# Optimization experiments

Measured on AMD Instinct MI355X. Metric: run time of the kernel, lower is better.

## Reference

```python
import jax, jax.numpy as jnp
import numpy as np

QUANT_DEPTH = 4
EMBED_DIM = 256
N_EMBED = 8192
B, H, W = 8, 32, 32


def setup_inputs() -> dict:
    key = jax.random.key(0)
    k1, k2 = jax.random.split(key)
    x = jax.random.normal(k1, (B, H, W, EMBED_DIM), dtype=jnp.float32)
    codebooks = jax.random.normal(k2, (QUANT_DEPTH, N_EMBED, EMBED_DIM), dtype=jnp.float32)
    return {"x": x, "codebooks": codebooks}


def _nearest_code(flat, cb):
    # flat: [N, D], cb: [K, D] -> idx: [N]
    # ||v - c||^2 = ||v||^2 + ||c||^2 - 2 v.c  (addmm in torch source)
    d = (jnp.sum(flat * flat, axis=1, keepdims=True)
         + jnp.sum(cb * cb, axis=1)[None, :]
         - 2.0 * (flat @ cb.T))  # [N, K]
    return jnp.argmin(d, axis=1)


def reference(x, codebooks):
    Bx, h, w, D = x.shape
    # quantization path is entirely non-differentiable (torch: detach + no_grad)
    resid = jax.lax.stop_gradient(x)
    agg = jnp.zeros_like(resid)
    quant_list = []
    code_list = []
    for i in range(codebooks.shape[0]):
        cb = codebooks[i]                      # [K, D]
        idx = _nearest_code(resid.reshape(-1, D), cb)  # [N]
        quant = cb[idx].reshape(Bx, h, w, D)
        resid = resid - quant
        agg = agg + quant
        quant_list.append(agg)
        code_list.append(idx.reshape(Bx, h, w, 1))
    codes = jnp.concatenate(code_list, axis=-1)  # [B, h, w, depth]
    # commitment loss: mean over depths of mean((x - agg_i.detach())^2)
    commitment_loss = jnp.mean(
        jnp.stack([jnp.mean((x - jax.lax.stop_gradient(q)) ** 2) for q in quant_list]))
    # straight-through estimator
    quants_trunc = x + jax.lax.stop_gradient(quant_list[-1] - x)
    return quants_trunc, commitment_loss, codes
```

## Files before the change

### kernel.cpp

```cpp
#include <hip/hip_runtime.h>

#define DIM   256
#define NVEC  8192
#define NCODE 8192
#define DEPTH 4

#define KBLK  8
#define KC    (NCODE / KBLK)
#define KT    (KC / 128)
#define FCAP  8192
#define FKS   32
#define FV    8
#define KAPPA 0.025f

typedef short  b8 __attribute__((ext_vector_type(8)));
typedef short  b4 __attribute__((ext_vector_type(4)));
typedef float  f4 __attribute__((ext_vector_type(4)));

static __device__ __forceinline__ unsigned short f2bf(float f) {
  unsigned u = __float_as_uint(f);
  return (unsigned short)((u + 0x7FFFu + ((u >> 16) & 1u)) >> 16);
}

static __device__ __forceinline__ void gll16(const void* g, void* l) {
  __builtin_amdgcn_global_load_lds(
      (const __attribute__((address_space(1))) void*)g,
      (__attribute__((address_space(3))) void*)l, 16, 0, 0);
}

__global__ __launch_bounds__(256) void prep_norms(const float* __restrict__ cb_all,
                                                  float* __restrict__ cc,
                                                  float* __restrict__ cchat) {
  int row  = blockIdx.x * 4 + (threadIdx.x >> 6);
  int lane = threadIdx.x & 63;
  float4 v = *(const float4*)&cb_all[(size_t)row * DIM + lane * 4];
  float st = 0.f, sh = 0.f;
  float vv[4] = {v.x, v.y, v.z, v.w};
  #pragma unroll
  for (int j = 0; j < 4; ++j) {
    float hf = __uint_as_float(((unsigned)f2bf(vv[j])) << 16);
    st += vv[j] * vv[j];
    sh += hf * hf;
  }
  #pragma unroll
  for (int off = 32; off > 0; off >>= 1) {
    st += __shfl_down(st, off, 64);
    sh += __shfl_down(sh, off, 64);
  }
  if (lane == 0) { cc[row] = st; cchat[row] = sh; }
}

__global__ __launch_bounds__(256) void prep_depth(const float* __restrict__ cbd,
                                                  unsigned short* __restrict__ cbh,
                                                  float* __restrict__ cbT) {
  __shared__ float ts[64][68];
  const int kb = blockIdx.x >> 2, db = blockIdx.x & 3;
  const int k0 = kb * 64, d0 = db * 64;
  const int t  = threadIdx.x;
  const int r  = t >> 2;
  const int c4 = (t & 3) * 16;

  const float* src = cbd + (size_t)(k0 + r) * DIM + d0 + c4;
  float4 q[4];
  #pragma unroll
  for (int i = 0; i < 4; ++i) q[i] = *(const float4*)(src + i * 4);

  b8 h0, h1;
  #pragma unroll
  for (int j = 0; j < 4; ++j) { h0[j] = (short)f2bf(q[0][j]); h0[4 + j] = (short)f2bf(q[1][j]); }
  #pragma unroll
  for (int j = 0; j < 4; ++j) { h1[j] = (short)f2bf(q[2][j]); h1[4 + j] = (short)f2bf(q[3][j]); }
  *(b8*)&cbh[(size_t)(k0 + r) * DIM + d0 + c4]     = h0;
  *(b8*)&cbh[(size_t)(k0 + r) * DIM + d0 + c4 + 8] = h1;

  #pragma unroll
  for (int i = 0; i < 4; ++i)
    #pragma unroll
    for (int j = 0; j < 4; ++j)
      ts[c4 + i * 4 + j][r] = q[i][j];
  __syncthreads();

  const int dd = t >> 2, kk4 = (t & 3) * 16;
  float* dst = cbT + (size_t)(d0 + dd) * NCODE + k0 + kk4;
  #pragma unroll
  for (int q4 = 0; q4 < 4; ++q4)
    *(float4*)(dst + q4 * 4) = *(const float4*)&ts[dd][kk4 + q4 * 4];
}

__global__ __launch_bounds__(256) void init_kernel(const float* __restrict__ x,
                                                   float* __restrict__ resid,
                                                   unsigned short* __restrict__ rb,
                                                   float* __restrict__ rsum0) {
  int n    = blockIdx.x * 4 + (threadIdx.x >> 6);
  int lane = threadIdx.x & 63;
  float4 v = *(const float4*)&x[(size_t)n * DIM + lane * 4];
  *(float4*)&resid[(size_t)n * DIM + lane * 4] = v;
  b4 hv; hv[0] = (short)f2bf(v.x); hv[1] = (short)f2bf(v.y);
  hv[2] = (short)f2bf(v.z); hv[3] = (short)f2bf(v.w);
  *(b4*)&rb[(size_t)n * DIM + lane * 4] = hv;
  float s = v.x * v.x + v.y * v.y + v.z * v.z + v.w * v.w;
  #pragma unroll
  for (int off = 32; off > 0; off >>= 1) s += __shfl_down(s, off, 64);
  if (lane == 0) rsum0[n] = s;
}

__global__ __launch_bounds__(512, 2) void coarse_kernel(
    const unsigned short* __restrict__ rb,
    const unsigned short* __restrict__ cbh,
    const float* __restrict__ cchat,
    float* __restrict__ pv1, int* __restrict__ pi1, float* __restrict__ pv2,
    int* __restrict__ fcount) {
  __shared__ __align__(16) char lds[53248];

  const int tid  = threadIdx.x;
  const int w    = tid >> 6;
  const int l    = tid & 63;
  const int mw   = w >> 1, kw = w & 1;
  const int mblk = blockIdx.x / KBLK;
  const int kblk = blockIdx.x % KBLK;
  const int m0   = mblk * 128;
  const int K0   = kblk * KC;

  if (blockIdx.x == 0 && tid == 0) *fcount = 0;

  int boff[2], ldst[2];
  #pragma unroll
  for (int it = 0; it < 2; ++it) {
    int o = it * 512 + tid;
    int row = o >> 3, ssl = (o & 7) ^ (row & 7);
    boff[it] = (K0 + row) * 512 + ssl * 16;
    ldst[it] = o * 16;
  }
  int offB[4][2];
  #pragma unroll
  for (int nf = 0; nf < 4; ++nf) {
    int row = kw * 64 + nf * 16 + (l & 15);
    int base = row * 128 + (((l >> 4) ^ (row & 7)) * 16);
    offB[nf][0] = base; offB[nf][1] = base ^ 64;
  }

  b8 ar[4][2][2];
  {
    const char* ab = (const char*)rb +
        (size_t)(m0 + mw * 32 + (l & 15)) * 512 + (l >> 4) * 16;
    #pragma unroll
    for (int dt = 0; dt < 4; ++dt)
      #pragma unroll
      for (int kk = 0; kk < 2; ++kk)
        #pragma unroll
        for (int mf = 0; mf < 2; ++mf)
          ar[dt][kk][mf] =
              *(const b8*)(ab + mf * (16 * 512) + dt * 128 + kk * 64);
  }
  if (tid < 256)
    gll16((const char*)cchat + (size_t)K0 * 4 + tid * 16,
          lds + 49152 + tid * 16);

  asm volatile("s_waitcnt vmcnt(0)");
  __builtin_amdgcn_sched_barrier(0);

  #pragma unroll
  for (int s = 0; s < 2; ++s)
    #pragma unroll
    for (int it = 0; it < 2; ++it)
      gll16((const char*)cbh + boff[it] + (s >> 2) * 65536 + (s & 3) * 128,
            lds + (s % 3) * 16384 + ldst[it]);

  const float* ccl = (const float*)(lds + 49152);
  const int kgb = K0 + kw * 64 + (l & 15);

  float tv1[8], tv2[8];
  int   ti1[8];
  #pragma unroll
  for (int s = 0; s < 8; ++s) { tv1[s] = 3.4e38f; tv2[s] = 3.4e38f; ti1[s] = 0; }

  f4 acc[2][4];

  #pragma unroll
  for (int p = 0; p < 32; ++p) {
    const int kt = p >> 2, dt = p & 3, cb_ = p % 3;
    if (p == 31) { asm volatile("s_waitcnt vmcnt(0)"); }
    else         { asm volatile("s_waitcnt vmcnt(2)"); }
    __builtin_amdgcn_s_barrier();
    __builtin_amdgcn_sched_barrier(0);
    if (p < 30) {
      const int s2 = p + 2, nb = s2 % 3, nkt = s2 >> 2, ndt = s2 & 3;
      #pragma unroll
      for (int it = 0; it < 2; ++it)
        gll16((const char*)cbh + boff[it] + nkt * 65536 + ndt * 128,
              lds + nb * 16384 + ldst[it]);
    }
    if (dt == 0) {
      #pragma unroll
      for (int i = 0; i < 2; ++i)
        #pragma unroll
        for (int j = 0; j < 4; ++j)
          acc[i][j] = (f4){0.f, 0.f, 0.f, 0.f};
    }
    __builtin_amdgcn_s_setprio(1);
    #pragma unroll
    for (int kk = 0; kk < 2; ++kk) {
      b8 bb[4];
      #pragma unroll
      for (int nf = 0; nf < 4; ++nf)
        bb[nf] = *(const b8*)(lds + cb_ * 16384 + offB[nf][kk]);
      #pragma unroll
      for (int mf = 0; mf < 2; ++mf)
        #pragma unroll
        for (int nf = 0; nf < 4; ++nf)
          acc[mf][nf] = __builtin_amdgcn_mfma_f32_16x16x32_bf16(
              ar[dt][kk][mf], bb[nf], acc[mf][nf], 0, 0, 0);
    }
    __builtin_amdgcn_s_setprio(0);
    if (dt == 3) {
      float cn[4]; int kg[4];
      #pragma unroll
      for (int nf = 0; nf < 4; ++nf) {
        kg[nf] = kgb + kt * 128 + nf * 16;
        cn[nf] = ccl[kt * 128 + kw * 64 + nf * 16 + (l & 15)];
      }
      #pragma unroll
      for (int mf = 0; mf < 2; ++mf)
        #pragma unroll
        for (int r = 0; r < 4; ++r) {
          const int s0 = mf * 4 + r;
          #pragma unroll
          for (int nf = 0; nf < 4; ++nf) {
            float s = fmaf(-2.f, acc[mf][nf][r], cn[nf]);
            bool  c = s < tv1[s0];
            float m2 = fminf(tv2[s0], s);
            tv2[s0] = c ? tv1[s0] : m2;
            ti1[s0] = c ? kg[nf] : ti1[s0];
            tv1[s0] = c ? s : tv1[s0];
          }
        }
    }
  }
  __syncthreads();

  float* Mv1 = (float*)lds;
  int*   Mi1 = (int*)(lds + 1024);
  float* Mv2 = (float*)(lds + 2048);

  #pragma unroll
  for (int s0 = 0; s0 < 8; ++s0) {
    float v1 = tv1[s0], v2 = tv2[s0];
    int   i1 = ti1[s0];
    #pragma unroll
    for (int m = 1; m < 16; m <<= 1) {
      float qv1 = __shfl_xor(v1, m);
      int   qi1 = __shfl_xor(i1, m);
      float qv2 = __shfl_xor(v2, m);
      bool  qw  = (qv1 < v1) || (qv1 == v1 && qi1 < i1);
      float lose = qw ? v1 : qv1;
      float wv2  = qw ? qv2 : v2;
      v2 = fminf(wv2, lose);
      if (qw) { v1 = qv1; i1 = qi1; }
    }
    if ((l & 15) == 0) {
      int mf = s0 >> 2, r = s0 & 3;
      int rowL = mw * 32 + mf * 16 + (l >> 4) * 4 + r;
      Mv1[rowL * 2 + kw] = v1; Mi1[rowL * 2 + kw] = i1; Mv2[rowL * 2 + kw] = v2;
    }
  }
  __syncthreads();
  if (tid < 128) {
    float a1 = Mv1[tid * 2],     a2 = Mv2[tid * 2];     int a1i = Mi1[tid * 2];
    float b1 = Mv1[tid * 2 + 1], b2 = Mv2[tid * 2 + 1]; int b1i = Mi1[tid * 2 + 1];
    bool  bw = (b1 < a1) || (b1 == a1 && b1i < a1i);
    float v1 = bw ? b1 : a1; int i1 = bw ? b1i : a1i;
    float v2 = fminf(bw ? b2 : a2, bw ? a1 : b1);
    int n = m0 + tid;
    pv1[kblk * NVEC + n] = v1;
    pi1[kblk * NVEC + n] = i1;
    pv2[kblk * NVEC + n] = v2;
  }
}

__global__ __launch_bounds__(256) void merge_kernel(
    const float* __restrict__ pv1, const int* __restrict__ pi1,
    const float* __restrict__ pv2, const float* __restrict__ vnorm,
    int* __restrict__ idx, int* __restrict__ flist, int* __restrict__ fslot,
    int* __restrict__ fcount) {
  int n = blockIdx.x * 256 + threadIdx.x;
  float v1 = 3.4e38f, v2 = 3.4e38f; int i1 = 0;
  #pragma unroll
  for (int kb = 0; kb < KBLK; ++kb) {
    float b1 = pv1[kb * NVEC + n]; int b1i = pi1[kb * NVEC + n];
    float b2 = pv2[kb * NVEC + n];
    bool  bw = (b1 < v1) || (b1 == v1 && b1i < i1);
    float lose = bw ? v1 : b1;
    float wv2  = bw ? b2 : v2;
    v2 = fminf(wv2, lose);
    if (bw) { v1 = b1; i1 = b1i; }
  }
  idx[n] = i1;
  float thr = KAPPA * sqrtf(fmaxf(v1 + vnorm[n], 0.f)) + 1e-5f;
  int slot = -1;
  if (v2 - v1 < thr) {
    slot = atomicAdd(fcount, 1);
    flist[slot] = n;
  }
  fslot[n] = slot;
}

__global__ __launch_bounds__(256, 4) void fb_scan_t(
    const float* __restrict__ cbT, const float* __restrict__ cc,
    const float* __restrict__ resid, const int* __restrict__ flist,
    const int* __restrict__ fcount,
    float* __restrict__ fpv, int* __restrict__ fpi) {
  __shared__ float vsT[DIM][FV + 4];
  __shared__ float mv[FV][4];
  __shared__ int   mi[FV][4];
  const int cnt = min(*fcount, FCAP);
  const int ks = blockIdx.x & (FKS - 1);
  const int t = threadIdx.x;
  const int w = t >> 6, l = t & 63;
  const int k = ks * 256 + t;
  const float cn = cc[k];

  for (int chunk = blockIdx.x >> 5; chunk * FV < cnt; chunk += 256) {
    __syncthreads();
    #pragma unroll
    for (int v = 0; v < FV; ++v) {
      int s = chunk * FV + v;
      int n = flist[s < cnt ? s : chunk * FV];
      vsT[t][v] = resid[(size_t)n * DIM + t];
    }
    __syncthreads();

    float dot[FV];
    #pragma unroll
    for (int v = 0; v < FV; ++v) dot[v] = 0.f;

    #pragma unroll 8
    for (int d = 0; d < DIM; ++d) {
      float cv = cbT[(size_t)d * NCODE + k];
      f4 a0 = *(const f4*)&vsT[d][0];
      f4 a1 = *(const f4*)&vsT[d][4];
      dot[0] = fmaf(cv, a0[0], dot[0]);
      dot[1] = fmaf(cv, a0[1], dot[1]);
      dot[2] = fmaf(cv, a0[2], dot[2]);
      dot[3] = fmaf(cv, a0[3], dot[3]);
      dot[4] = fmaf(cv, a1[0], dot[4]);
      dot[5] = fmaf(cv, a1[1], dot[5]);
      dot[6] = fmaf(cv, a1[2], dot[6]);
      dot[7] = fmaf(cv, a1[3], dot[7]);
    }

    #pragma unroll
    for (int v = 0; v < FV; ++v) {
      float bv = fmaf(-2.f, dot[v], cn);
      int   bi = k;
      #pragma unroll
      for (int m = 1; m < 64; m <<= 1) {
        float qv = __shfl_xor(bv, m);
        int   qi = __shfl_xor(bi, m);
        if (qv < bv || (qv == bv && qi < bi)) { bv = qv; bi = qi; }
      }
      if (l == 0) { mv[v][w] = bv; mi[v][w] = bi; }
    }
    __syncthreads();
    if (t < FV) {
      float bv = mv[t][0]; int bi = mi[t][0];
      #pragma unroll
      for (int ww = 1; ww < 4; ++ww) {
        float qv = mv[t][ww]; int qi = mi[t][ww];
        if (qv < bv || (qv == bv && qi < bi)) { bv = qv; bi = qi; }
      }
      if (chunk * FV + t < cnt) {
        fpv[(size_t)(chunk * FV + t) * FKS + ks] = bv;
        fpi[(size_t)(chunk * FV + t) * FKS + ks] = bi;
      }
    }
  }
}

__global__ __launch_bounds__(256) void update_kernel(
    const float* __restrict__ cb, const int* __restrict__ idx,
    const int* __restrict__ fslot,
    const float* __restrict__ fpv, const int* __restrict__ fpi,
    float* __restrict__ resid, unsigned short* __restrict__ rb,
    float* __restrict__ rsum_out, float* __restrict__ codes_out, int depth) {
  int n    = blockIdx.x * 4 + (threadIdx.x >> 6);
  int lane = threadIdx.x & 63;
  int s    = fslot[n];
  int bi;
  if (s >= 0) {
    float v = 3.4e38f; int ii = 0x7fffffff;
    if (lane < FKS) { v = fpv[(size_t)s * FKS + lane]; ii = fpi[(size_t)s * FKS + lane]; }
    #pragma unroll
    for (int m = 1; m < FKS; m <<= 1) {
      float qv = __shfl_xor(v, m);
      int   qi = __shfl_xor(ii, m);
      if (qv < v || (qv == v && qi < ii)) { v = qv; ii = qi; }
    }
    bi = __shfl(ii, 0, 64);
  } else {
    bi = idx[n];
  }
  float4 q = *(const float4*)&cb[(size_t)bi * DIM + lane * 4];
  float4 r = *(float4*)&resid[(size_t)n * DIM + lane * 4];
  r.x -= q.x; r.y -= q.y; r.z -= q.z; r.w -= q.w;
  *(float4*)&resid[(size_t)n * DIM + lane * 4] = r;
  b4 hv; hv[0] = (short)f2bf(r.x); hv[1] = (short)f2bf(r.y);
  hv[2] = (short)f2bf(r.z); hv[3] = (short)f2bf(r.w);
  *(b4*)&rb[(size_t)n * DIM + lane * 4] = hv;
  float s2 = r.x * r.x + r.y * r.y + r.z * r.z + r.w * r.w;
  #pragma unroll
  for (int off = 32; off > 0; off >>= 1) s2 += __shfl_down(s2, off, 64);
  if (lane == 0) {
    rsum_out[n] = s2;
    codes_out[n * DEPTH + depth] = (float)bi;
  }
}

__global__ __launch_bounds__(256) void finalize(const float* __restrict__ x,
                                                float* __restrict__ out,
                                                const float* __restrict__ rsumL) {
  int i = blockIdx.x * blockDim.x + threadIdx.x;
  float4 r  = *(float4*)&out[(size_t)i * 4];
  float4 xv = *(const float4*)&x[(size_t)i * 4];
  float4 o;
  o.x = xv.x - r.x; o.y = xv.y - r.y; o.z = xv.z - r.z; o.w = xv.w - r.w;
  *(float4*)&out[(size_t)i * 4] = o;

  if (blockIdx.x == 0) {
    __shared__ float sm[256];
    float s = 0.f;
    for (int j = threadIdx.x; j < DEPTH * NVEC; j += 256) s += rsumL[j];
    sm[threadIdx.x] = s;
    __syncthreads();
    for (int off = 128; off > 0; off >>= 1) {
      if (threadIdx.x < off) sm[threadIdx.x] += sm[threadIdx.x + off];
      __syncthreads();
    }
    if (threadIdx.x == 0)
      out[NVEC * DIM] = sm[0] / (float)DEPTH / (float)(NVEC * DIM);
  }
}

extern "C" void kernel_launch(void* const* d_in, const int* in_sizes, int n_in,
                              void* d_out, int out_size, void* d_ws, size_t ws_size,
                              hipStream_t stream) {
  const float* x  = (const float*)d_in[0];
  const float* cb = (const float*)d_in[1];
  float* out = (float*)d_out;
  char*  wsb = (char*)d_ws;

  unsigned short* cbh = (unsigned short*)(wsb);
  unsigned short* rb  = (unsigned short*)(wsb + 4194304);
  float* cbT   = (float*)(wsb + 8388608);
  float* cc    = (float*)(wsb + 16777216);
  float* cchat = (float*)(wsb + 16908288);
  float* pv1   = (float*)(wsb + 17039360);
  int*   pi1   = (int*)  (wsb + 17563648);
  float* pv2   = (float*)(wsb + 18087936);
  float* rsum  = (float*)(wsb + 18612224);
  int*   idx   = (int*)  (wsb + 18776064);
  int*   flist = (int*)  (wsb + 18808832);
  int*   fslot = (int*)  (wsb + 18841600);
  int*   fcount= (int*)  (wsb + 18874368);
  float* fpv   = (float*)(wsb + 18878464);
  int*   fpi   = (int*)  (wsb + 19927040);

  float* resid     = out;
  float* codes_out = out + NVEC * DIM + 1;

  prep_norms<<<(DEPTH * NCODE) / 4, 256, 0, stream>>>(cb, cc, cchat);
  init_kernel<<<NVEC / 4, 256, 0, stream>>>(x, resid, rb, rsum);

  for (int d = 0; d < DEPTH; ++d) {
    const size_t cbo = (size_t)d * NCODE * DIM;
    prep_depth<<<512, 256, 0, stream>>>(cb + cbo, cbh, cbT);
    coarse_kernel<<<(NVEC / 128) * KBLK, 512, 0, stream>>>(
        rb, cbh, cchat + d * NCODE, pv1, pi1, pv2, fcount);
    merge_kernel<<<NVEC / 256, 256, 0, stream>>>(
        pv1, pi1, pv2, rsum + d * NVEC, idx, flist, fslot, fcount);
    fb_scan_t<<<256 * FKS, 256, 0, stream>>>(
        cbT, cc + d * NCODE, resid, flist, fcount, fpv, fpi);
    update_kernel<<<NVEC / 4, 256, 0, stream>>>(
        cb + cbo, idx, fslot, fpv, fpi, resid, rb,
        rsum + (d + 1) * NVEC, codes_out, d);
  }
  finalize<<<(NVEC * DIM / 4) / 256, 256, 0, stream>>>(x, out, rsum + NVEC);
}
```

Measured before the change: 513.8 us.

## Restructure coarse GEMM pipeline to 4-buffer LDS ring, tighten fallback margin and grid

The coarse bf16 MFMA kernel moves from a 3-slot LDS ring with a barrier before each stage to a 4-slot ring. LDS B-fragment reads for a stage are issued before the next global-to-LDS prefetch and the barrier, so LDS latency overlaps the wait. The top-2 tracking now uses fmed3/fmin in place of compare-select. The fallback margin KAPPA is lowered so fewer vectors go to the exact fp32 rescan, and the fallback grid is halved (FCH=128 chunks). Together these aim to cut synchronisation stalls and fallback work, but the larger LDS footprint may limit occupancy and the tighter margin risks misidentifying nearest codes.

```diff
diff --git a/kernel.cpp b/kernel.cpp
--- a/kernel.cpp
+++ b/kernel.cpp
@@ -11,7 +11,8 @@
 #define FCAP  8192
 #define FKS   32
 #define FV    8
-#define KAPPA 0.025f
+#define FCH   128
+#define KAPPA 0.018f
 
 typedef short  b8 __attribute__((ext_vector_type(8)));
 typedef short  b4 __attribute__((ext_vector_type(4)));
@@ -110,7 +111,7 @@
     const float* __restrict__ cchat,
     float* __restrict__ pv1, int* __restrict__ pi1, float* __restrict__ pv2,
     int* __restrict__ fcount) {
-  __shared__ __align__(16) char lds[53248];
+  __shared__ __align__(16) char lds[69632];
 
   const int tid  = threadIdx.x;
   const int w    = tid >> 6;
@@ -138,6 +139,7 @@
     int base = row * 128 + (((l >> 4) ^ (row & 7)) * 16);
     offB[nf][0] = base; offB[nf][1] = base ^ 64;
   }
+  const int kgb = K0 + kw * 64 + (l & 15);
 
   b8 ar[4][2][2];
   {
@@ -153,21 +155,23 @@
               *(const b8*)(ab + mf * (16 * 512) + dt * 128 + kk * 64);
   }
   if (tid < 256)
-    gll16((const char*)cchat + (size_t)K0 * 4 + tid * 16,
-          lds + 49152 + tid * 16);
+    gll16((const char*)cchat + (size_t)K0 * 4 + tid * 16, lds + 65536 + tid * 16);
 
   asm volatile("s_waitcnt vmcnt(0)");
   __builtin_amdgcn_sched_barrier(0);
 
   #pragma unroll
-  for (int s = 0; s < 2; ++s)
-    #pragma unroll
-    for (int it = 0; it < 2; ++it)
-      gll16((const char*)cbh + boff[it] + (s >> 2) * 65536 + (s & 3) * 128,
-            lds + (s % 3) * 16384 + ldst[it]);
-
-  const float* ccl = (const float*)(lds + 49152);
-  const int kgb = K0 + kw * 64 + (l & 15);
+  for (int it = 0; it < 2; ++it)
+    gll16((const char*)cbh + boff[it], lds + ldst[it]);
+  #pragma unroll
+  for (int it = 0; it < 2; ++it)
+    gll16((const char*)cbh + boff[it] + 128, lds + 16384 + ldst[it]);
+  asm volatile("s_waitcnt vmcnt(2)");
+  __builtin_amdgcn_sched_barrier(0);
+  __builtin_amdgcn_s_barrier();
+  __builtin_amdgcn_sched_barrier(0);
+
+  const float* ccl = (const float*)(lds + 65536);
 
   float tv1[8], tv2[8];
   int   ti1[8];
@@ -176,64 +180,72 @@
 
   f4 acc[2][4];
 
-  #pragma unroll
-  for (int p = 0; p < 32; ++p) {
-    const int kt = p >> 2, dt = p & 3, cb_ = p % 3;
-    if (p == 31) { asm volatile("s_waitcnt vmcnt(0)"); }
-    else         { asm volatile("s_waitcnt vmcnt(2)"); }
-    __builtin_amdgcn_s_barrier();
-    __builtin_amdgcn_sched_barrier(0);
-    if (p < 30) {
-      const int s2 = p + 2, nb = s2 % 3, nkt = s2 >> 2, ndt = s2 & 3;
-      #pragma unroll
-      for (int it = 0; it < 2; ++it)
-        gll16((const char*)cbh + boff[it] + nkt * 65536 + ndt * 128,
-              lds + nb * 16384 + ldst[it]);
-    }
-    if (dt == 0) {
-      #pragma unroll
-      for (int i = 0; i < 2; ++i)
-        #pragma unroll
-        for (int j = 0; j < 4; ++j)
-          acc[i][j] = (f4){0.f, 0.f, 0.f, 0.f};
-    }
-    __builtin_amdgcn_s_setprio(1);
-    #pragma unroll
-    for (int kk = 0; kk < 2; ++kk) {
-      b8 bb[4];
+  for (int kt = 0; kt < KT; ++kt) {
+    #pragma unroll
+    for (int dt = 0; dt < 4; ++dt) {
+      b8 bb[4][2];
       #pragma unroll
       for (int nf = 0; nf < 4; ++nf)
-        bb[nf] = *(const b8*)(lds + cb_ * 16384 + offB[nf][kk]);
+        #pragma unroll
+        for (int kk = 0; kk < 2; ++kk)
+          bb[nf][kk] = *(const b8*)(lds + dt * 16384 + offB[nf][kk]);
+      if (!(kt == KT - 1 && dt >= 2)) {
+        const int skt = (dt >= 2) ? kt + 1 : kt;
+        const int sdt = (dt + 2) & 3;
+        #pragma unroll
+        for (int it = 0; it < 2; ++it)
+          gll16((const char*)cbh + boff[it] + skt * 65536 + sdt * 128,
+                lds + ((dt + 2) & 3) * 16384 + ldst[it]);
+      }
+      if (!(kt == KT - 1 && dt >= 2)) {
+        asm volatile("s_waitcnt vmcnt(2)");
+      } else if (dt == 2) {
+        asm volatile("s_waitcnt vmcnt(0)");
+      }
+      __builtin_amdgcn_sched_barrier(0);
+      __builtin_amdgcn_s_barrier();
+      __builtin_amdgcn_sched_barrier(0);
+      asm volatile("s_waitcnt lgkmcnt(0)");
+      __builtin_amdgcn_sched_barrier(0);
+      if (dt == 0) {
+        #pragma unroll
+        for (int i = 0; i < 2; ++i)
+          #pragma unroll
+          for (int j = 0; j < 4; ++j)
+            acc[i][j] = (f4){0.f, 0.f, 0.f, 0.f};
+      }
+      __builtin_amdgcn_s_setprio(1);
       #pragma unroll
-      for (int mf = 0; mf < 2; ++mf)
-        #pragma unroll
-        for (int nf = 0; nf < 4; ++nf)
-          acc[mf][nf] = __builtin_amdgcn_mfma_f32_16x16x32_bf16(
-              ar[dt][kk][mf], bb[nf], acc[mf][nf], 0, 0, 0);
-    }
-    __builtin_amdgcn_s_setprio(0);
-    if (dt == 3) {
-      float cn[4]; int kg[4];
-      #pragma unroll
-      for (int nf = 0; nf < 4; ++nf) {
-        kg[nf] = kgb + kt * 128 + nf * 16;
-        cn[nf] = ccl[kt * 128 + kw * 64 + nf * 16 + (l & 15)];
-      }
-      #pragma unroll
-      for (int mf = 0; mf < 2; ++mf)
-        #pragma unroll
-        for (int r = 0; r < 4; ++r) {
-          const int s0 = mf * 4 + r;
+      for (int kk = 0; kk < 2; ++kk)
+        #pragma unroll
+        for (int mf = 0; mf < 2; ++mf)
           #pragma unroll
-          for (int nf = 0; nf < 4; ++nf) {
-            float s = fmaf(-2.f, acc[mf][nf][r], cn[nf]);
-            bool  c = s < tv1[s0];
-            float m2 = fminf(tv2[s0], s);
-            tv2[s0] = c ? tv1[s0] : m2;
-            ti1[s0] = c ? kg[nf] : ti1[s0];
-            tv1[s0] = c ? s : tv1[s0];
+          for (int nf = 0; nf < 4; ++nf)
+            acc[mf][nf] = __builtin_amdgcn_mfma_f32_16x16x32_bf16(
+                ar[dt][kk][mf], bb[nf][kk], acc[mf][nf], 0, 0, 0);
+      __builtin_amdgcn_s_setprio(0);
+      if (dt == 3) {
+        float cn[4]; int kg[4];
+        #pragma unroll
+        for (int nf = 0; nf < 4; ++nf) {
+          kg[nf] = kgb + kt * 128 + nf * 16;
+          cn[nf] = ccl[kt * 128 + kw * 64 + nf * 16 + (l & 15)];
+        }
+        #pragma unroll
+        for (int mf = 0; mf < 2; ++mf)
+          #pragma unroll
+          for (int r = 0; r < 4; ++r) {
+            const int s0 = mf * 4 + r;
+            #pragma unroll
+            for (int nf = 0; nf < 4; ++nf) {
+              float s = fmaf(-2.f, acc[mf][nf][r], cn[nf]);
+              bool  c = s < tv1[s0];
+              tv2[s0] = __builtin_amdgcn_fmed3f(s, tv1[s0], tv2[s0]);
+              ti1[s0] = c ? kg[nf] : ti1[s0];
+              tv1[s0] = fminf(tv1[s0], s);
+            }
           }
-        }
+      }
     }
   }
   __syncthreads();
@@ -319,7 +331,7 @@
   const int k = ks * 256 + t;
   const float cn = cc[k];
 
-  for (int chunk = blockIdx.x >> 5; chunk * FV < cnt; chunk += 256) {
+  for (int chunk = blockIdx.x >> 5; chunk * FV < cnt; chunk += FCH) {
     __syncthreads();
     #pragma unroll
     for (int v = 0; v < FV; ++v) {
@@ -477,7 +489,7 @@
         rb, cbh, cchat + d * NCODE, pv1, pi1, pv2, fcount);
     merge_kernel<<<NVEC / 256, 256, 0, stream>>>(
         pv1, pi1, pv2, rsum + d * NVEC, idx, flist, fslot, fcount);
-    fb_scan_t<<<256 * FKS, 256, 0, stream>>>(
+    fb_scan_t<<<FCH * FKS, 256, 0, stream>>>(
         cbT, cc + d * NCODE, resid, flist, fcount, fpv, fpi);
     update_kernel<<<NVEC / 4, 256, 0, stream>>>(
         cb + cbo, idx, fslot, fpv, fpi, resid, rb,
```

Result: faster. 447.4 us (-12.9%).
